# Optimization experiments

Measured on AMD Instinct MI355X. Metric: run time of the kernel, lower is better.

The kernel has to match this reference:

```python
import jax, jax.numpy as jnp
from jax import lax
import numpy as np

VOCAB, EMB, HID = 32000, 512, 1024
B, T = 64, 512


def setup_inputs() -> dict:
    key = jax.random.key(0)
    ks = jax.random.split(key, 12)
    s = 0.05
    return {
        "x": jax.random.randint(ks[0], (B, T), 0, VOCAB),
        "lengths": jax.random.randint(ks[1], (B,), 0, T),
        "emb_table": jax.random.normal(ks[2], (VOCAB, EMB), jnp.float32) * s,
        "W_ih": jax.random.normal(ks[3], (4 * HID, EMB), jnp.float32) * s,
        "b_ih": jax.random.normal(ks[4], (4 * HID,), jnp.float32) * s,
        "W_hh": jax.random.normal(ks[5], (4 * HID, HID), jnp.float32) * s,
        "b_hh": jax.random.normal(ks[6], (4 * HID,), jnp.float32) * s,
        "W1": jax.random.normal(ks[7], (64, HID), jnp.float32) * s,
        "b1": jax.random.normal(ks[8], (64,), jnp.float32) * s,
        "W2": jax.random.normal(ks[9], (1, 64), jnp.float32) * s,
        "b2": jax.random.normal(ks[10], (1,), jnp.float32) * s,
    }


def reference(x, lengths, emb_table, W_ih, b_ih, W_hh, b_hh, W1, b1, W2, b2):
    # padding_idx=0 -> embedding row 0 is zeros
    emb_table = emb_table.at[0].set(0.0)
    emb = emb_table[x]                                   # [B, T, EMB]
    # Precompute the input projection for all timesteps (one big GEMM),
    # mathematically identical to doing it per-step inside LSTMCell.
    x_proj = jnp.einsum("btd,gd->btg", emb, W_ih) + b_ih  # [B, T, 4H]
    xs = jnp.swapaxes(x_proj, 0, 1)                       # [T, B, 4H]

    h0 = jnp.zeros((x.shape[0], HID), emb.dtype)
    c0 = jnp.zeros((x.shape[0], HID), emb.dtype)

    def step(carry, x_t):
        h, c = carry
        gates = x_t + h @ W_hh.T + b_hh                   # [B, 4H]
        i, f, g, o = jnp.split(gates, 4, axis=-1)         # torch gate order: i,f,g,o
        c = jax.nn.sigmoid(f) * c + jax.nn.sigmoid(i) * jnp.tanh(g)
        h = jax.nn.sigmoid(o) * jnp.tanh(c)
        return (h, c), None

    (h_T, _), _ = lax.scan(step, (h0, c0), xs)

    hidden = jax.nn.relu(h_T @ W1.T + b1)                 # [B, 64]
    out = hidden @ W2.T + b2                              # [B, 1]
    return out.squeeze(-1)                                # [B]
```

## Files before the change

### kernel.cpp

```cpp
#include <hip/hip_runtime.h>
#include <stdint.h>
#include <math.h>


#define HID  1024
#define EMBD 512
#define NB   64
#define NT   512
#define G4   4096

using bf16x8  = __attribute__((ext_vector_type(8))) __bf16;
using ushort8 = __attribute__((ext_vector_type(8))) unsigned short;
using f32x4   = __attribute__((ext_vector_type(4))) float;

__device__ __forceinline__ unsigned short f2bf(float f) {
  unsigned u = __float_as_uint(f);
  u += 0x7fffu + ((u >> 16) & 1u);
  return (unsigned short)(u >> 16);
}
__device__ __forceinline__ float bf2f(unsigned short s) {
  return __uint_as_float(((unsigned)s) << 16);
}

__global__ void prep_weights(const float* __restrict__ Wih, const float* __restrict__ Whh,
                             unsigned short* __restrict__ WihHi, unsigned short* __restrict__ WihLo,
                             unsigned short* __restrict__ WhhHi, unsigned short* __restrict__ WhhLo) {
  const int NIH = G4 * EMBD;
  int idx = blockIdx.x * 256 + threadIdx.x;
  if (idx < NIH) {
    float v = Wih[idx];
    unsigned short hb = f2bf(v);
    WihHi[idx] = hb;
    WihLo[idx] = f2bf(v - bf2f(hb));
  } else {
    int k = idx - NIH;
    float v = Whh[k];
    unsigned short hb = f2bf(v);
    WhhHi[k] = hb;
    WhhLo[k] = f2bf(v - bf2f(hb));
  }
}

__global__ void prep_bias(const float* __restrict__ bih, const float* __restrict__ bhh,
                          float* __restrict__ bias) {
  int i = blockIdx.x * 256 + threadIdx.x;
  if (i < G4) bias[i] = bih[i] + bhh[i];
}

__global__ void zero_state(float* __restrict__ c,
                           unsigned short* __restrict__ hHi0,
                           unsigned short* __restrict__ hLo0) {
  int i = blockIdx.x * 256 + threadIdx.x;
  c[i] = 0.f;
  hHi0[i] = 0;
  hLo0[i] = 0;
}

__global__ __launch_bounds__(256) void lstm_step(
    const int* __restrict__ x, const float* __restrict__ emb,
    const unsigned short* __restrict__ WihHi, const unsigned short* __restrict__ WihLo,
    const unsigned short* __restrict__ WhhHi, const unsigned short* __restrict__ WhhLo,
    const float* __restrict__ bias,
    const unsigned short* __restrict__ hHiIn, const unsigned short* __restrict__ hLoIn,
    unsigned short* __restrict__ hHiOut, unsigned short* __restrict__ hLoOut,
    float* __restrict__ c, int t) {
  const int wg   = blockIdx.x;
  const int bt   = wg >> 7;
  const int gt   = wg & 127;
  const int tid  = threadIdx.x;
  const int wave = tid >> 6;
  const int lane = tid & 63;
  const int msub = wave >> 1, nsub = wave & 1;
  const int l15  = lane & 15;
  const int kg8  = (lane >> 4) * 8;

  const int mrow = bt * 32 + msub * 16 + l15;
  const int nloc = nsub * 16 + l15;
  const int grow = (nloc >> 3) * HID + gt * 8 + (nloc & 7);

  f32x4 acc = {0.f, 0.f, 0.f, 0.f};

  const int  tok = x[mrow * NT + t];
  const bool pad = (tok == 0);
  const float* erow = emb + (size_t)tok * EMBD;

  {
    const unsigned short* bH = WihHi + (size_t)grow * EMBD;
    const unsigned short* bL = WihLo + (size_t)grow * EMBD;
#pragma unroll 4
    for (int kc = 0; kc < 16; ++kc) {
      const int k0 = kc * 32 + kg8;
      ushort8 ah, al;
#pragma unroll
      for (int i = 0; i < 8; ++i) {
        float v = pad ? 0.f : erow[k0 + i];
        unsigned short hb = f2bf(v);
        ah[i] = hb;
        al[i] = f2bf(v - bf2f(hb));
      }
      bf16x8 aH = __builtin_bit_cast(bf16x8, ah);
      bf16x8 aL = __builtin_bit_cast(bf16x8, al);
      bf16x8 bHf = *(const bf16x8*)(bH + k0);
      bf16x8 bLf = *(const bf16x8*)(bL + k0);
      acc = __builtin_amdgcn_mfma_f32_16x16x32_bf16(aH, bHf, acc, 0, 0, 0);
      acc = __builtin_amdgcn_mfma_f32_16x16x32_bf16(aH, bLf, acc, 0, 0, 0);
      acc = __builtin_amdgcn_mfma_f32_16x16x32_bf16(aL, bHf, acc, 0, 0, 0);
    }
  }
  {
    const unsigned short* aHp = hHiIn + (size_t)mrow * HID;
    const unsigned short* aLp = hLoIn + (size_t)mrow * HID;
    const unsigned short* bHp = WhhHi + (size_t)grow * HID;
    const unsigned short* bLp = WhhLo + (size_t)grow * HID;
#pragma unroll 4
    for (int kc = 0; kc < 32; ++kc) {
      const int k0 = kc * 32 + kg8;
      bf16x8 aHf = *(const bf16x8*)(aHp + k0);
      bf16x8 aLf = *(const bf16x8*)(aLp + k0);
      bf16x8 bHf = *(const bf16x8*)(bHp + k0);
      bf16x8 bLf = *(const bf16x8*)(bLp + k0);
      acc = __builtin_amdgcn_mfma_f32_16x16x32_bf16(aHf, bHf, acc, 0, 0, 0);
      acc = __builtin_amdgcn_mfma_f32_16x16x32_bf16(aHf, bLf, acc, 0, 0, 0);
      acc = __builtin_amdgcn_mfma_f32_16x16x32_bf16(aLf, bHf, acc, 0, 0, 0);
    }
  }

  __shared__ float gl[32][33];
  const int mb = msub * 16 + (lane >> 4) * 4;
#pragma unroll
  for (int r = 0; r < 4; ++r) gl[nloc][mb + r] = acc[r];
  __syncthreads();

  const int bl = tid >> 3;
  const int j  = tid & 7;
  const int hu = gt * 8 + j;
  const int bglob = bt * 32 + bl;
  const int cidx  = bglob * HID + hu;

  float gi = gl[0 + j][bl]  + bias[hu];
  float gf = gl[8 + j][bl]  + bias[HID + hu];
  float gg = gl[16 + j][bl] + bias[2 * HID + hu];
  float go = gl[24 + j][bl] + bias[3 * HID + hu];

  float si = 1.f / (1.f + expf(-gi));
  float sf = 1.f / (1.f + expf(-gf));
  float so = 1.f / (1.f + expf(-go));
  float tg = tanhf(gg);
  float cn = sf * c[cidx] + si * tg;
  float hn = so * tanhf(cn);
  c[cidx] = cn;
  unsigned short hb = f2bf(hn);
  hHiOut[cidx] = hb;
  hLoOut[cidx] = f2bf(hn - bf2f(hb));
}

__global__ __launch_bounds__(256) void head_kernel(
    const unsigned short* __restrict__ hHi, const unsigned short* __restrict__ hLo,
    const float* __restrict__ W1, const float* __restrict__ b1,
    const float* __restrict__ W2, const float* __restrict__ b2,
    float* __restrict__ out) {
  const int b = blockIdx.x;
  const int tid = threadIdx.x;
  const int u = tid >> 2, q = tid & 3;
  const int base = b * HID;

  float s = 0.f;
  const int k0 = q * 256;
#pragma unroll 4
  for (int k = k0; k < k0 + 256; ++k) {
    float hv = bf2f(hHi[base + k]) + bf2f(hLo[base + k]);
    s += W1[u * HID + k] * hv;
  }
  __shared__ float red[64][4];
  __shared__ float hl[64];
  red[u][q] = s;
  __syncthreads();
  if (tid < 64) {
    float v = red[tid][0] + red[tid][1] + red[tid][2] + red[tid][3] + b1[tid];
    hl[tid] = v > 0.f ? v : 0.f;
  }
  __syncthreads();
  if (tid < 64) {
    float v = hl[tid] * W2[tid];
#pragma unroll
    for (int off = 32; off; off >>= 1) v += __shfl_down(v, off);
    if (tid == 0) out[b] = v + b2[0];
  }
}

extern "C" void kernel_launch(void* const* d_in, const int* in_sizes, int n_in,
                              void* d_out, int out_size, void* d_ws, size_t ws_size,
                              hipStream_t stream) {
  const int*   x   = (const int*)d_in[0];
  const float* emb = (const float*)d_in[2];
  const float* Wih = (const float*)d_in[3];
  const float* bih = (const float*)d_in[4];
  const float* Whh = (const float*)d_in[5];
  const float* bhh = (const float*)d_in[6];
  const float* W1  = (const float*)d_in[7];
  const float* b1  = (const float*)d_in[8];
  const float* W2  = (const float*)d_in[9];
  const float* b2  = (const float*)d_in[10];
  float* out = (float*)d_out;

  char* ws = (char*)d_ws;
  float*          c     = (float*)(ws + 0);
  unsigned short* hHi   = (unsigned short*)(ws + (256 << 10));
  unsigned short* hLo   = (unsigned short*)(ws + (512 << 10));
  float*          bias  = (float*)(ws + (768 << 10));
  unsigned short* WihHi = (unsigned short*)(ws + (784 << 10));
  unsigned short* WihLo = WihHi + (size_t)G4 * EMBD;
  unsigned short* WhhHi = WihLo + (size_t)G4 * EMBD;
  unsigned short* WhhLo = WhhHi + (size_t)G4 * HID;
  const size_t ws_needed = (784ull << 10) + 2ull * ((size_t)G4 * EMBD + (size_t)G4 * HID) * 2ull * 2ull;
  if (ws_size < ws_needed) return;

  zero_state<<<256, 256, 0, stream>>>(c, hHi, hLo);
  prep_bias<<<16, 256, 0, stream>>>(bih, bhh, bias);
  prep_weights<<<(G4 * EMBD + G4 * HID) / 256, 256, 0, stream>>>(Wih, Whh, WihHi, WihLo, WhhHi, WhhLo);

  for (int t = 0; t < NT; ++t) {
    const unsigned short* hiIn = hHi + (size_t)(t & 1) * (NB * HID);
    const unsigned short* loIn = hLo + (size_t)(t & 1) * (NB * HID);
    unsigned short* hiOut = hHi + (size_t)((t + 1) & 1) * (NB * HID);
    unsigned short* loOut = hLo + (size_t)((t + 1) & 1) * (NB * HID);
    lstm_step<<<256, 256, 0, stream>>>(x, emb, WihHi, WihLo, WhhHi, WhhLo, bias,
                                       hiIn, loIn, hiOut, loOut, c, t);
  }
  head_kernel<<<64, 256, 0, stream>>>(hHi, hLo, W1, b1, W2, b2, out);
}
```

Measured before the change: 18.59 ms.

## Replace per-timestep launches with persistent cooperative LSTM kernel using LDS-resident weights

After: 39.30 ms. 111% more time.

```diff
diff --git a/kernel.cpp b/kernel.cpp
--- a/kernel.cpp
+++ b/kernel.cpp
@@ -1,4 +1,5 @@
 #include <hip/hip_runtime.h>
+#include <hip/hip_cooperative_groups.h>
 #include <stdint.h>
 #include <math.h>
 
@@ -8,6 +9,8 @@
 #define NB   64
 #define NT   512
 #define G4   4096
+#define NWG  256
+#define TPB  256
 
 using bf16x8  = __attribute__((ext_vector_type(8))) __bf16;
 using ushort8 = __attribute__((ext_vector_type(8))) unsigned short;
@@ -22,23 +25,8 @@
   return __uint_as_float(((unsigned)s) << 16);
 }
 
-__global__ void prep_weights(const float* __restrict__ Wih, const float* __restrict__ Whh,
-                             unsigned short* __restrict__ WihHi, unsigned short* __restrict__ WihLo,
-                             unsigned short* __restrict__ WhhHi, unsigned short* __restrict__ WhhLo) {
-  const int NIH = G4 * EMBD;
-  int idx = blockIdx.x * 256 + threadIdx.x;
-  if (idx < NIH) {
-    float v = Wih[idx];
-    unsigned short hb = f2bf(v);
-    WihHi[idx] = hb;
-    WihLo[idx] = f2bf(v - bf2f(hb));
-  } else {
-    int k = idx - NIH;
-    float v = Whh[k];
-    unsigned short hb = f2bf(v);
-    WhhHi[k] = hb;
-    WhhLo[k] = f2bf(v - bf2f(hb));
-  }
+__global__ void zero_state(unsigned int* __restrict__ p) {
+  p[blockIdx.x * 256 + threadIdx.x] = 0u;
 }
 
 __global__ void prep_bias(const float* __restrict__ bih, const float* __restrict__ bhh,
@@ -47,111 +35,174 @@
   if (i < G4) bias[i] = bih[i] + bhh[i];
 }
 
-__global__ void zero_state(float* __restrict__ c,
-                           unsigned short* __restrict__ hHi0,
-                           unsigned short* __restrict__ hLo0) {
-  int i = blockIdx.x * 256 + threadIdx.x;
-  c[i] = 0.f;
-  hHi0[i] = 0;
-  hLo0[i] = 0;
-}
-
-__global__ __launch_bounds__(256) void lstm_step(
+__global__ void prep_emb(const int* __restrict__ x, const float* __restrict__ emb,
+                         unsigned short* __restrict__ eHi, unsigned short* __restrict__ eLo) {
+  const int bid = blockIdx.x;
+  const int b = bid & (NB - 1);
+  const int t = bid >> 6;
+  const int k = threadIdx.x * 4;
+  const int tok = x[b * NT + t];
+  float4 v = {0.f, 0.f, 0.f, 0.f};
+  if (tok != 0) v = *(const float4*)(emb + (size_t)tok * EMBD + k);
+  float vs[4] = {v.x, v.y, v.z, v.w};
+  unsigned short hs[4], ls[4];
+#pragma unroll
+  for (int i = 0; i < 4; ++i) {
+    unsigned short hb = f2bf(vs[i]);
+    hs[i] = hb;
+    ls[i] = f2bf(vs[i] - bf2f(hb));
+  }
+  const size_t base = (size_t)bid * EMBD + k;
+  *(uint2*)(eHi + base) = make_uint2((unsigned)hs[0] | ((unsigned)hs[1] << 16),
+                                     (unsigned)hs[2] | ((unsigned)hs[3] << 16));
+  *(uint2*)(eLo + base) = make_uint2((unsigned)ls[0] | ((unsigned)ls[1] << 16),
+                                     (unsigned)ls[2] | ((unsigned)ls[3] << 16));
+}
+
+__global__ __launch_bounds__(TPB, 1) void lstm_persistent(
     const int* __restrict__ x, const float* __restrict__ emb,
-    const unsigned short* __restrict__ WihHi, const unsigned short* __restrict__ WihLo,
-    const unsigned short* __restrict__ WhhHi, const unsigned short* __restrict__ WhhLo,
+    const unsigned short* __restrict__ eHi, const unsigned short* __restrict__ eLo,
+    const int embSplit,
+    const float* __restrict__ Wih, const float* __restrict__ Whh,
     const float* __restrict__ bias,
-    const unsigned short* __restrict__ hHiIn, const unsigned short* __restrict__ hLoIn,
-    unsigned short* __restrict__ hHiOut, unsigned short* __restrict__ hLoOut,
-    float* __restrict__ c, int t) {
-  const int wg   = blockIdx.x;
-  const int bt   = wg >> 7;
-  const int gt   = wg & 127;
+    unsigned short* __restrict__ h0Hi, unsigned short* __restrict__ h0Lo,
+    unsigned short* __restrict__ h1Hi, unsigned short* __restrict__ h1Lo) {
+  extern __shared__ unsigned short wb[];
+  unsigned short* wbHi = wb;
+  unsigned short* wbLo = wb + 24576;
+  __shared__ float gl[16][68];
+  __shared__ unsigned short hst[64][8];
+
+  const int gt   = blockIdx.x;
   const int tid  = threadIdx.x;
+  const int lane = tid & 63;
   const int wave = tid >> 6;
-  const int lane = tid & 63;
-  const int msub = wave >> 1, nsub = wave & 1;
-  const int l15  = lane & 15;
+
+  for (int e = tid; e < 24576; e += TPB) {
+    const int i = e & 7, n = (e >> 3) & 15, kg = (e >> 7) & 3, kc = e >> 9;
+    const int k = kc * 32 + kg * 8 + i;
+    const int grow = (n >> 2) * HID + gt * 4 + (n & 3);
+    const float v = (k < EMBD) ? Wih[(size_t)grow * EMBD + k]
+                               : Whh[(size_t)grow * HID + (k - EMBD)];
+    const unsigned short hb = f2bf(v);
+    wbHi[e] = hb;
+    wbLo[e] = f2bf(v - bf2f(hb));
+  }
+
+  const int cb = tid >> 2, cj = tid & 3;
+  const int hu = gt * 4 + cj;
+  const float bI = bias[hu], bF = bias[HID + hu];
+  const float bG = bias[2 * HID + hu], bO = bias[3 * HID + hu];
+  float c_reg = 0.f;
+
+  const int m15  = lane & 15;
   const int kg8  = (lane >> 4) * 8;
-
-  const int mrow = bt * 32 + msub * 16 + l15;
-  const int nloc = nsub * 16 + l15;
-  const int grow = (nloc >> 3) * HID + gt * 8 + (nloc & 7);
-
-  f32x4 acc = {0.f, 0.f, 0.f, 0.f};
-
-  const int  tok = x[mrow * NT + t];
-  const bool pad = (tok == 0);
-  const float* erow = emb + (size_t)tok * EMBD;
-
-  {
-    const unsigned short* bH = WihHi + (size_t)grow * EMBD;
-    const unsigned short* bL = WihLo + (size_t)grow * EMBD;
+  const int mrow = wave * 16 + m15;
+
+  cooperative_groups::grid_group grid = cooperative_groups::this_grid();
+  __syncthreads();
+
+  for (int t = 0; t < NT; ++t) {
+    const unsigned short* hInHi = (t & 1) ? h1Hi : h0Hi;
+    const unsigned short* hInLo = (t & 1) ? h1Lo : h0Lo;
+    unsigned short* hOutHi = (t & 1) ? h0Hi : h1Hi;
+    unsigned short* hOutLo = (t & 1) ? h0Lo : h1Lo;
+
+    f32x4 acc0 = {0.f, 0.f, 0.f, 0.f}, acc1 = {0.f, 0.f, 0.f, 0.f};
+
+    if (embSplit) {
+      const unsigned short* eh = eHi + ((size_t)t * NB + mrow) * EMBD;
+      const unsigned short* el = eLo + ((size_t)t * NB + mrow) * EMBD;
 #pragma unroll 4
-    for (int kc = 0; kc < 16; ++kc) {
-      const int k0 = kc * 32 + kg8;
-      ushort8 ah, al;
-#pragma unroll
-      for (int i = 0; i < 8; ++i) {
-        float v = pad ? 0.f : erow[k0 + i];
-        unsigned short hb = f2bf(v);
-        ah[i] = hb;
-        al[i] = f2bf(v - bf2f(hb));
+      for (int kc = 0; kc < 16; ++kc) {
+        const int k0 = kc * 32 + kg8;
+        bf16x8 aH = *(const bf16x8*)(eh + k0);
+        bf16x8 aL = *(const bf16x8*)(el + k0);
+        bf16x8 bH = *(const bf16x8*)(wbHi + kc * 512 + lane * 8);
+        bf16x8 bL = *(const bf16x8*)(wbLo + kc * 512 + lane * 8);
+        f32x4& acc = (kc & 1) ? acc1 : acc0;
+        acc = __builtin_amdgcn_mfma_f32_16x16x32_bf16(aH, bH, acc, 0, 0, 0);
+        acc = __builtin_amdgcn_mfma_f32_16x16x32_bf16(aH, bL, acc, 0, 0, 0);
+        acc = __builtin_amdgcn_mfma_f32_16x16x32_bf16(aL, bH, acc, 0, 0, 0);
       }
-      bf16x8 aH = __builtin_bit_cast(bf16x8, ah);
-      bf16x8 aL = __builtin_bit_cast(bf16x8, al);
-      bf16x8 bHf = *(const bf16x8*)(bH + k0);
-      bf16x8 bLf = *(const bf16x8*)(bL + k0);
-      acc = __builtin_amdgcn_mfma_f32_16x16x32_bf16(aH, bHf, acc, 0, 0, 0);
-      acc = __builtin_amdgcn_mfma_f32_16x16x32_bf16(aH, bLf, acc, 0, 0, 0);
-      acc = __builtin_amdgcn_mfma_f32_16x16x32_bf16(aL, bHf, acc, 0, 0, 0);
+    } else {
+      const int tok = x[mrow * NT + t];
+      const float* erow = emb + (size_t)tok * EMBD;
+#pragma unroll 2
+      for (int kc = 0; kc < 16; ++kc) {
+        const int k0 = kc * 32 + kg8;
+        float4 f0 = {0.f, 0.f, 0.f, 0.f}, f1 = {0.f, 0.f, 0.f, 0.f};
+        if (tok != 0) {
+          f0 = *(const float4*)(erow + k0);
+          f1 = *(const float4*)(erow + k0 + 4);
+        }
+        const float vs[8] = {f0.x, f0.y, f0.z, f0.w, f1.x, f1.y, f1.z, f1.w};
+        ushort8 ah, al;
+#pragma unroll
+        for (int i = 0; i < 8; ++i) {
+          unsigned short hb = f2bf(vs[i]);
+          ah[i] = hb;
+          al[i] = f2bf(vs[i] - bf2f(hb));
+        }
+        bf16x8 aH = __builtin_bit_cast(bf16x8, ah);
+        bf16x8 aL = __builtin_bit_cast(bf16x8, al);
+        bf16x8 bH = *(const bf16x8*)(wbHi + kc * 512 + lane * 8);
+        bf16x8 bL = *(const bf16x8*)(wbLo + kc * 512 + lane * 8);
+        f32x4& acc = (kc & 1) ? acc1 : acc0;
+        acc = __builtin_amdgcn_mfma_f32_16x16x32_bf16(aH, bH, acc, 0, 0, 0);
+        acc = __builtin_amdgcn_mfma_f32_16x16x32_bf16(aH, bL, acc, 0, 0, 0);
+        acc = __builtin_amdgcn_mfma_f32_16x16x32_bf16(aL, bH, acc, 0, 0, 0);
+      }
     }
-  }
-  {
-    const unsigned short* aHp = hHiIn + (size_t)mrow * HID;
-    const unsigned short* aLp = hLoIn + (size_t)mrow * HID;
-    const unsigned short* bHp = WhhHi + (size_t)grow * HID;
-    const unsigned short* bLp = WhhLo + (size_t)grow * HID;
+
+    {
+      const unsigned short* ah_ = hInHi + (size_t)mrow * HID;
+      const unsigned short* al_ = hInLo + (size_t)mrow * HID;
 #pragma unroll 4
-    for (int kc = 0; kc < 32; ++kc) {
-      const int k0 = kc * 32 + kg8;
-      bf16x8 aHf = *(const bf16x8*)(aHp + k0);
-      bf16x8 aLf = *(const bf16x8*)(aLp + k0);
-      bf16x8 bHf = *(const bf16x8*)(bHp + k0);
-      bf16x8 bLf = *(const bf16x8*)(bLp + k0);
-      acc = __builtin_amdgcn_mfma_f32_16x16x32_bf16(aHf, bHf, acc, 0, 0, 0);
-      acc = __builtin_amdgcn_mfma_f32_16x16x32_bf16(aHf, bLf, acc, 0, 0, 0);
-      acc = __builtin_amdgcn_mfma_f32_16x16x32_bf16(aLf, bHf, acc, 0, 0, 0);
+      for (int kc = 0; kc < 32; ++kc) {
+        const int k0 = kc * 32 + kg8;
+        bf16x8 aH = *(const bf16x8*)(ah_ + k0);
+        bf16x8 aL = *(const bf16x8*)(al_ + k0);
+        bf16x8 bH = *(const bf16x8*)(wbHi + (16 + kc) * 512 + lane * 8);
+        bf16x8 bL = *(const bf16x8*)(wbLo + (16 + kc) * 512 + lane * 8);
+        f32x4& acc = (kc & 1) ? acc1 : acc0;
+        acc = __builtin_amdgcn_mfma_f32_16x16x32_bf16(aH, bH, acc, 0, 0, 0);
+        acc = __builtin_amdgcn_mfma_f32_16x16x32_bf16(aH, bL, acc, 0, 0, 0);
+        acc = __builtin_amdgcn_mfma_f32_16x16x32_bf16(aL, bH, acc, 0, 0, 0);
+      }
     }
-  }
-
-  __shared__ float gl[32][33];
-  const int mb = msub * 16 + (lane >> 4) * 4;
-#pragma unroll
-  for (int r = 0; r < 4; ++r) gl[nloc][mb + r] = acc[r];
-  __syncthreads();
-
-  const int bl = tid >> 3;
-  const int j  = tid & 7;
-  const int hu = gt * 8 + j;
-  const int bglob = bt * 32 + bl;
-  const int cidx  = bglob * HID + hu;
-
-  float gi = gl[0 + j][bl]  + bias[hu];
-  float gf = gl[8 + j][bl]  + bias[HID + hu];
-  float gg = gl[16 + j][bl] + bias[2 * HID + hu];
-  float go = gl[24 + j][bl] + bias[3 * HID + hu];
-
-  float si = 1.f / (1.f + expf(-gi));
-  float sf = 1.f / (1.f + expf(-gf));
-  float so = 1.f / (1.f + expf(-go));
-  float tg = tanhf(gg);
-  float cn = sf * c[cidx] + si * tg;
-  float hn = so * tanhf(cn);
-  c[cidx] = cn;
-  unsigned short hb = f2bf(hn);
-  hHiOut[cidx] = hb;
-  hLoOut[cidx] = f2bf(hn - bf2f(hb));
+
+    const int mb = wave * 16 + (lane >> 4) * 4;
+#pragma unroll
+    for (int r = 0; r < 4; ++r) gl[m15][mb + r] = acc0[r] + acc1[r];
+    __syncthreads();
+
+    const float gi = gl[0 + cj][cb] + bI;
+    const float gf = gl[4 + cj][cb] + bF;
+    const float gg = gl[8 + cj][cb] + bG;
+    const float go = gl[12 + cj][cb] + bO;
+    const float si = 1.f / (1.f + expf(-gi));
+    const float sf = 1.f / (1.f + expf(-gf));
+    const float so = 1.f / (1.f + expf(-go));
+    const float tg = tanhf(gg);
+    c_reg = sf * c_reg + si * tg;
+    const float hn = so * tanhf(c_reg);
+    const unsigned short hb = f2bf(hn);
+    hst[cb][cj] = hb;
+    hst[cb][4 + cj] = f2bf(hn - bf2f(hb));
+    __syncthreads();
+
+    if (tid < 64) {
+      const unsigned long long v = *(const unsigned long long*)&hst[tid][0];
+      *(unsigned long long*)(hOutHi + (size_t)tid * HID + gt * 4) = v;
+    } else if (tid < 128) {
+      const int b = tid - 64;
+      const unsigned long long v = *(const unsigned long long*)&hst[b][4];
+      *(unsigned long long*)(hOutLo + (size_t)b * HID + gt * 4) = v;
+    }
+    __threadfence();
+    grid.sync();
+  }
 }
 
 __global__ __launch_bounds__(256) void head_kernel(
@@ -191,6 +242,7 @@
 extern "C" void kernel_launch(void* const* d_in, const int* in_sizes, int n_in,
                               void* d_out, int out_size, void* d_ws, size_t ws_size,
                               hipStream_t stream) {
+  (void)in_sizes; (void)n_in; (void)out_size;
   const int*   x   = (const int*)d_in[0];
   const float* emb = (const float*)d_in[2];
   const float* Wih = (const float*)d_in[3];
@@ -204,28 +256,32 @@
   float* out = (float*)d_out;
 
   char* ws = (char*)d_ws;
-  float*          c     = (float*)(ws + 0);
-  unsigned short* hHi   = (unsigned short*)(ws + (256 << 10));
-  unsigned short* hLo   = (unsigned short*)(ws + (512 << 10));
-  float*          bias  = (float*)(ws + (768 << 10));
-  unsigned short* WihHi = (unsigned short*)(ws + (784 << 10));
-  unsigned short* WihLo = WihHi + (size_t)G4 * EMBD;
-  unsigned short* WhhHi = WihLo + (size_t)G4 * EMBD;
-  unsigned short* WhhLo = WhhHi + (size_t)G4 * HID;
-  const size_t ws_needed = (784ull << 10) + 2ull * ((size_t)G4 * EMBD + (size_t)G4 * HID) * 2ull * 2ull;
-  if (ws_size < ws_needed) return;
-
-  zero_state<<<256, 256, 0, stream>>>(c, hHi, hLo);
+  unsigned short* h0Hi = (unsigned short*)(ws);
+  unsigned short* h0Lo = (unsigned short*)(ws + (128 << 10));
+  unsigned short* h1Hi = (unsigned short*)(ws + (256 << 10));
+  unsigned short* h1Lo = (unsigned short*)(ws + (384 << 10));
+  float*          bias = (float*)(ws + (512 << 10));
+  unsigned short* eHi  = (unsigned short*)(ws + (528 << 10));
+  unsigned short* eLo  = eHi + (size_t)NB * NT * EMBD;
+
+  const size_t need_min  = (528ull << 10);
+  const size_t need_full = need_min + 2ull * ((size_t)NB * NT * EMBD * 2);
+  if (ws_size < need_min) return;
+  int embSplit = (ws_size >= need_full) ? 1 : 0;
+
+  const unsigned dynLDS = 2u * 24576u * 2u;
+  (void)hipFuncSetAttribute((const void*)lstm_persistent,
+                            hipFuncAttributeMaxDynamicSharedMemorySize, (int)dynLDS);
+
+  zero_state<<<256, 256, 0, stream>>>((unsigned int*)ws);
   prep_bias<<<16, 256, 0, stream>>>(bih, bhh, bias);
-  prep_weights<<<(G4 * EMBD + G4 * HID) / 256, 256, 0, stream>>>(Wih, Whh, WihHi, WihLo, WhhHi, WhhLo);
-
-  for (int t = 0; t < NT; ++t) {
-    const unsigned short* hiIn = hHi + (size_t)(t & 1) * (NB * HID);
-    const unsigned short* loIn = hLo + (size_t)(t & 1) * (NB * HID);
-    unsigned short* hiOut = hHi + (size_t)((t + 1) & 1) * (NB * HID);
-    unsigned short* loOut = hLo + (size_t)((t + 1) & 1) * (NB * HID);
-    lstm_step<<<256, 256, 0, stream>>>(x, emb, WihHi, WihLo, WhhHi, WhhLo, bias,
-                                       hiIn, loIn, hiOut, loOut, c, t);
-  }
-  head_kernel<<<64, 256, 0, stream>>>(hHi, hLo, W1, b1, W2, b2, out);
-}
+  if (embSplit) prep_emb<<<NB * NT, 128, 0, stream>>>(x, emb, eHi, eLo);
+
+  void* args[] = {(void*)&x, (void*)&emb, (void*)&eHi, (void*)&eLo, (void*)&embSplit,
+                  (void*)&Wih, (void*)&Whh, (void*)&bias,
+                  (void*)&h0Hi, (void*)&h0Lo, (void*)&h1Hi, (void*)&h1Lo};
+  (void)hipLaunchCooperativeKernel((void*)lstm_persistent, dim3(NWG), dim3(TPB),
+                                   args, dynLDS, stream);
+
+  head_kernel<<<64, 256, 0, stream>>>(h0Hi, h0Lo, W1, b1, W2, b2, out);
+}
```
